# Kernel optimization log

Measured on AMD Instinct MI355X. Metric: run time of the kernel, lower is better.

The kernel has to match this reference:

```python
import jax, jax.numpy as jnp
from jax import lax
import numpy as np

B, T, D, H, K = 16, 2048, 512, 512, 2

def setup_inputs() -> dict:
    key = jax.random.key(0)
    k1, k2, k3 = jax.random.split(key, 3)
    inputs = jax.random.normal(k1, (B, T, D), dtype=jnp.float32)
    conv_w = jax.random.normal(k2, (3 * H, D, K), dtype=jnp.float32) * (1.0 / np.sqrt(D * K))
    conv_b = jax.random.normal(k3, (3 * H,), dtype=jnp.float32) * 0.01
    return {"inputs": inputs, "conv_w": conv_w, "conv_b": conv_b}

def reference(inputs, conv_w, conv_b):
    # inputs: [B, T, D]; conv_w: [3H, D, K]; causal conv via left-pad K-1
    k = conv_w.shape[-1]
    h = conv_w.shape[0] // 3
    x = jnp.transpose(inputs, (0, 2, 1))                      # [B, D, T]
    x = jnp.pad(x, ((0, 0), (0, 0), (k - 1, 0)))              # left pad
    gates = lax.conv_general_dilated(
        x, conv_w, window_strides=(1,), padding='VALID',
        dimension_numbers=('NCH', 'OIH', 'NCH'))              # [B, 3H, T]
    gates = jnp.transpose(gates, (0, 2, 1)) + conv_b          # [B, T, 3H]
    Z, F, O = jnp.split(gates, 3, axis=2)
    Z = jnp.tanh(Z)
    F = jax.nn.sigmoid(F)
    O = jax.nn.sigmoid(O)

    # fo-pool: c_t = f_t * c_{t-1} + (1 - f_t) * z_t, c_{-1} = 0
    def step(c, zf):
        z, f = zf
        c_ = f * c + (1.0 - f) * z
        return c_, c_

    c0 = jnp.zeros((Z.shape[0], h), dtype=Z.dtype)
    _, C = lax.scan(step, c0, (jnp.swapaxes(Z, 0, 1), jnp.swapaxes(F, 0, 1)))
    C = jnp.swapaxes(C, 0, 1)                                 # [B, T, H]
    return C, O * C
```

## Files before the change

### kernel.cpp

```cpp
#include <hip/hip_runtime.h>


#define MTOT 32768
#define NTOT 1536
#define KTOT 1024
#define DCH  512
#define TLEN 2048
#define NB   16

#define HT 32
#define SC 8
#define LC 256

typedef __bf16 bf16x8 __attribute__((ext_vector_type(8)));
typedef float  f32x4  __attribute__((ext_vector_type(4)));

__device__ __forceinline__ unsigned short f2bf(float x) {
    unsigned u = __float_as_uint(x);
    u += 0x7FFFu + ((u >> 16) & 1u);
    return (unsigned short)(u >> 16);
}
__device__ __forceinline__ float bf2f(unsigned short h) {
    return __uint_as_float(((unsigned)h) << 16);
}
__device__ __forceinline__ float sigmoidf_(float x) {
    return 1.f / (1.f + __expf(-x));
}

__global__ __launch_bounds__(256) void make_A(const float* __restrict__ in,
                                              unsigned short* __restrict__ A) {
    size_t i = (size_t)blockIdx.x * 256 + threadIdx.x;
    size_t e = i * 8;
    size_t m = e >> 10;
    int    j = (int)(e & 1023);
    alignas(16) unsigned short h[8];
    if (((m & (TLEN - 1)) == 0) && (j < DCH)) {
#pragma unroll
        for (int r = 0; r < 8; ++r) h[r] = 0;
    } else {
        const float* src = in + ((long long)m - 1) * DCH + j;
        float4 a = *(const float4*)src;
        float4 b = *(const float4*)(src + 4);
        h[0] = f2bf(a.x); h[1] = f2bf(a.y); h[2] = f2bf(a.z); h[3] = f2bf(a.w);
        h[4] = f2bf(b.x); h[5] = f2bf(b.y); h[6] = f2bf(b.z); h[7] = f2bf(b.w);
    }
    *(int4*)(A + e) = *(const int4*)h;
}

__global__ __launch_bounds__(256) void make_B(const float* __restrict__ w,
                                              unsigned short* __restrict__ Bt) {
    int i = blockIdx.x * 256 + threadIdx.x;
    int o = i >> 9, d = i & 511;
    float w0 = w[(size_t)(o * 512 + d) * 2];
    float w1 = w[(size_t)(o * 512 + d) * 2 + 1];
    Bt[(size_t)o * 1024 + d]       = f2bf(w0);
    Bt[(size_t)o * 1024 + 512 + d] = f2bf(w1);
}

__global__ __launch_bounds__(256) void gemm_gates(const unsigned short* __restrict__ A,
                                                  const unsigned short* __restrict__ B,
                                                  const float* __restrict__ bias,
                                                  unsigned short* __restrict__ GT) {
    __shared__ int4 sA[512];
    __shared__ int4 sB[512];

    const int tid = threadIdx.x;
    const int bx  = blockIdx.x;
    const int mT  = bx / 12, nT = bx % 12;
    const int m0  = mT * 128, n0 = nT * 128;

    const int mloc = tid >> 2;
    const int qsw  = (tid & 3) ^ ((mloc >> 1) & 3);
    const unsigned short* ga0 = A + (size_t)(m0 + mloc) * 1024 + qsw * 8;
    const unsigned short* ga1 = A + (size_t)(m0 + 64 + mloc) * 1024 + qsw * 8;
    const unsigned short* gb0 = B + (size_t)(n0 + mloc) * 1024 + qsw * 8;
    const unsigned short* gb1 = B + (size_t)(n0 + 64 + mloc) * 1024 + qsw * 8;

    char* la0 = (char*)sA + tid * 16;
    char* la1 = (char*)sA + 4096 + tid * 16;
    char* lb0 = (char*)sB + tid * 16;
    char* lb1 = (char*)sB + 4096 + tid * 16;

    const int lane = tid & 63;
    const int wv   = tid >> 6;
    const int wm   = (wv & 1) * 64, wn = (wv >> 1) * 64;
    const int lr   = lane & 15, lq = lane >> 4;

    int sAidx[4], sBidx[4];
#pragma unroll
    for (int i = 0; i < 4; ++i) {
        int mi = wm + 16 * i + lr;
        sAidx[i] = mi * 4 + (lq ^ ((mi >> 1) & 3));
        int ni = wn + 16 * i + lr;
        sBidx[i] = ni * 4 + (lq ^ ((ni >> 1) & 3));
    }

    f32x4 acc[4][4] = {};

    for (int kt = 0; kt < KTOT; kt += 32) {
        __builtin_amdgcn_global_load_lds(
            (__attribute__((address_space(1))) void*)(void*)ga0,
            (__attribute__((address_space(3))) void*)la0, 16, 0, 0);
        __builtin_amdgcn_global_load_lds(
            (__attribute__((address_space(1))) void*)(void*)ga1,
            (__attribute__((address_space(3))) void*)la1, 16, 0, 0);
        __builtin_amdgcn_global_load_lds(
            (__attribute__((address_space(1))) void*)(void*)gb0,
            (__attribute__((address_space(3))) void*)lb0, 16, 0, 0);
        __builtin_amdgcn_global_load_lds(
            (__attribute__((address_space(1))) void*)(void*)gb1,
            (__attribute__((address_space(3))) void*)lb1, 16, 0, 0);
        ga0 += 32; ga1 += 32; gb0 += 32; gb1 += 32;
        __syncthreads();

        bf16x8 af[4], bfr[4];
#pragma unroll
        for (int i = 0; i < 4; ++i) af[i]  = __builtin_bit_cast(bf16x8, sA[sAidx[i]]);
#pragma unroll
        for (int j = 0; j < 4; ++j) bfr[j] = __builtin_bit_cast(bf16x8, sB[sBidx[j]]);

#pragma unroll
        for (int i = 0; i < 4; ++i)
#pragma unroll
            for (int j = 0; j < 4; ++j)
                acc[i][j] = __builtin_amdgcn_mfma_f32_16x16x32_bf16(af[i], bfr[j],
                                                                    acc[i][j], 0, 0, 0);
        __syncthreads();
    }

#pragma unroll
    for (int j = 0; j < 4; ++j) {
        int gn = n0 + wn + 16 * j + lr;
        float bj = bias[gn];
#pragma unroll
        for (int i = 0; i < 4; ++i) {
            int rowb = m0 + wm + 16 * i + lq * 4;
            alignas(8) unsigned short pk[4];
#pragma unroll
            for (int r = 0; r < 4; ++r) pk[r] = f2bf(acc[i][j][r] + bj);
            *(int2*)(GT + (size_t)gn * MTOT + rowb) = *(const int2*)pk;
        }
    }
}

__global__ __launch_bounds__(256) void scan_fo(const unsigned short* __restrict__ GT,
                                               float* __restrict__ out) {
    __shared__ float lP[SC][HT];
    __shared__ float lC[SC][HT];
    __shared__ float lI[SC][HT];

    const int tid   = threadIdx.x;
    const int h_loc = tid & (HT - 1);
    const int s     = tid >> 5;
    const int b     = blockIdx.x >> 4;
    const int h0    = (blockIdx.x & 15) * HT;
    const int h     = h0 + h_loc;

    const size_t mbase = (size_t)b * TLEN + (size_t)s * LC;
    const unsigned short* gz = GT + (size_t)h * MTOT + mbase;
    const unsigned short* gf = GT + (size_t)(DCH + h) * MTOT + mbase;
    const unsigned short* go = GT + (size_t)(2 * DCH + h) * MTOT + mbase;

    float P = 1.f, c = 0.f;
    for (int k = 0; k < LC; k += 8) {
        bf16x8 zv = *(const bf16x8*)(gz + k);
        bf16x8 fv = *(const bf16x8*)(gf + k);
#pragma unroll
        for (int r = 0; r < 8; ++r) {
            float f = sigmoidf_((float)fv[r]);
            float z = 2.f * sigmoidf_(2.f * (float)zv[r]) - 1.f;
            c = f * c + (1.f - f) * z;
            P *= f;
        }
    }
    lP[s][h_loc] = P;
    lC[s][h_loc] = c;
    __syncthreads();

    if (tid < HT) {
        float cc = 0.f;
#pragma unroll
        for (int ss = 0; ss < SC; ++ss) {
            lI[ss][tid] = cc;
            cc = lP[ss][tid] * cc + lC[ss][tid];
        }
    }
    __syncthreads();

    c = lI[s][h_loc];
    const size_t BTH = (size_t)NB * TLEN * DCH;
    float* oC  = out + mbase * DCH + h;
    float* oOC = oC + BTH;
    for (int k = 0; k < LC; k += 8) {
        bf16x8 zv = *(const bf16x8*)(gz + k);
        bf16x8 fv = *(const bf16x8*)(gf + k);
        bf16x8 ov = *(const bf16x8*)(go + k);
#pragma unroll
        for (int r = 0; r < 8; ++r) {
            float f = sigmoidf_((float)fv[r]);
            float z = 2.f * sigmoidf_(2.f * (float)zv[r]) - 1.f;
            float o = sigmoidf_((float)ov[r]);
            c = f * c + (1.f - f) * z;
            oC[(size_t)(k + r) * DCH]  = c;
            oOC[(size_t)(k + r) * DCH] = o * c;
        }
    }
}

extern "C" void kernel_launch(void* const* d_in, const int* in_sizes, int n_in,
                              void* d_out, int out_size, void* d_ws, size_t ws_size,
                              hipStream_t stream) {
    const float* in   = (const float*)d_in[0];
    const float* w    = (const float*)d_in[1];
    const float* bias = (const float*)d_in[2];
    float* out = (float*)d_out;

    unsigned short* Abf = (unsigned short*)d_ws;
    unsigned short* Bbf = Abf + (size_t)MTOT * 1024;
    unsigned short* GT  = Bbf + (size_t)NTOT * 1024;

    make_A<<<dim3(16384), dim3(256), 0, stream>>>(in, Abf);
    make_B<<<dim3(3072),  dim3(256), 0, stream>>>(w, Bbf);
    gemm_gates<<<dim3(3072), dim3(256), 0, stream>>>(Abf, Bbf, bias, GT);
    scan_fo<<<dim3(NB * (DCH / HT)), dim3(256), 0, stream>>>(GT, out);
}
```

Measured before the change: 407.7 us.

## Split fo-pool scan into three kernels with shorter chunks and remap GEMM blocks

The single scan kernel used 256 blocks, each walking 256-step chunks. It is replaced by three kernels: per-chunk prefix products and states over 64-step chunks (1024 blocks), a cross-chunk carry scan over 32 chunks per chain, and a final pass that writes the outputs. The point is more parallelism and shorter serial dependency chains in the recurrence, paid for with two extra launches and a small workspace round-trip. The workspace reuses the bf16 A buffer, which is dead once the GEMM finishes. The GEMM block index is also permuted so that neighbouring blocks land on different tile groups, which may change L2 locality.

```diff
diff --git a/kernel.cpp b/kernel.cpp
--- a/kernel.cpp
+++ b/kernel.cpp
@@ -8,9 +8,9 @@
 #define TLEN 2048
 #define NB   16
 
-#define HT 32
-#define SC 8
-#define LC 256
+#define LC2    64
+#define NCH    32
+#define CHAINS 8192
 
 typedef __bf16 bf16x8 __attribute__((ext_vector_type(8)));
 typedef float  f32x4  __attribute__((ext_vector_type(4)));
@@ -65,7 +65,8 @@
     __shared__ int4 sB[512];
 
     const int tid = threadIdx.x;
-    const int bx  = blockIdx.x;
+    const int bx0 = blockIdx.x;
+    const int bx  = (bx0 & 7) * 384 + (bx0 >> 3);
     const int mT  = bx / 12, nT = bx % 12;
     const int m0  = mT * 128, n0 = nT * 128;
 
@@ -143,26 +144,25 @@
     }
 }
 
-__global__ __launch_bounds__(256) void scan_fo(const unsigned short* __restrict__ GT,
-                                               float* __restrict__ out) {
-    __shared__ float lP[SC][HT];
-    __shared__ float lC[SC][HT];
-    __shared__ float lI[SC][HT];
-
+__global__ __launch_bounds__(256) void scan_part1(const unsigned short* __restrict__ GT,
+                                                  float* __restrict__ Pws,
+                                                  float* __restrict__ Cws) {
     const int tid   = threadIdx.x;
-    const int h_loc = tid & (HT - 1);
-    const int s     = tid >> 5;
-    const int b     = blockIdx.x >> 4;
-    const int h0    = (blockIdx.x & 15) * HT;
-    const int h     = h0 + h_loc;
-
-    const size_t mbase = (size_t)b * TLEN + (size_t)s * LC;
+    const int h_loc = tid & 31;
+    const int sc    = tid >> 5;
+    const int bid   = blockIdx.x;
+    const int tg    = bid & 3;
+    const int hg    = (bid >> 2) & 15;
+    const int b     = bid >> 6;
+    const int h     = hg * 32 + h_loc;
+    const int cg    = tg * 8 + sc;
+
+    const size_t mbase = (size_t)b * TLEN + (size_t)cg * LC2;
     const unsigned short* gz = GT + (size_t)h * MTOT + mbase;
     const unsigned short* gf = GT + (size_t)(DCH + h) * MTOT + mbase;
-    const unsigned short* go = GT + (size_t)(2 * DCH + h) * MTOT + mbase;
 
     float P = 1.f, c = 0.f;
-    for (int k = 0; k < LC; k += 8) {
+    for (int k = 0; k < LC2; k += 8) {
         bf16x8 zv = *(const bf16x8*)(gz + k);
         bf16x8 fv = *(const bf16x8*)(gf + k);
 #pragma unroll
@@ -173,25 +173,49 @@
             P *= f;
         }
     }
-    lP[s][h_loc] = P;
-    lC[s][h_loc] = c;
-    __syncthreads();
-
-    if (tid < HT) {
-        float cc = 0.f;
-#pragma unroll
-        for (int ss = 0; ss < SC; ++ss) {
-            lI[ss][tid] = cc;
-            cc = lP[ss][tid] * cc + lC[ss][tid];
-        }
-    }
-    __syncthreads();
-
-    c = lI[s][h_loc];
+    const int ch = b * DCH + h;
+    Pws[(size_t)cg * CHAINS + ch] = P;
+    Cws[(size_t)cg * CHAINS + ch] = c;
+}
+
+__global__ __launch_bounds__(256) void scan_part2(const float* __restrict__ Pws,
+                                                  const float* __restrict__ Cws,
+                                                  float* __restrict__ Iws) {
+    const int ch = blockIdx.x * 256 + threadIdx.x;
+    float cc = 0.f;
+#pragma unroll
+    for (int cg = 0; cg < NCH; ++cg) {
+        size_t idx = (size_t)cg * CHAINS + ch;
+        Iws[idx] = cc;
+        cc = Pws[idx] * cc + Cws[idx];
+    }
+}
+
+__global__ __launch_bounds__(256) void scan_part3(const unsigned short* __restrict__ GT,
+                                                  const float* __restrict__ Iws,
+                                                  float* __restrict__ out) {
+    const int tid   = threadIdx.x;
+    const int h_loc = tid & 31;
+    const int sc    = tid >> 5;
+    const int bid   = blockIdx.x;
+    const int tg    = bid & 3;
+    const int hg    = (bid >> 2) & 15;
+    const int b     = bid >> 6;
+    const int h     = hg * 32 + h_loc;
+    const int cg    = tg * 8 + sc;
+
+    const size_t mbase = (size_t)b * TLEN + (size_t)cg * LC2;
+    const unsigned short* gz = GT + (size_t)h * MTOT + mbase;
+    const unsigned short* gf = GT + (size_t)(DCH + h) * MTOT + mbase;
+    const unsigned short* go = GT + (size_t)(2 * DCH + h) * MTOT + mbase;
+
+    const int ch = b * DCH + h;
+    float c = Iws[(size_t)cg * CHAINS + ch];
+
     const size_t BTH = (size_t)NB * TLEN * DCH;
     float* oC  = out + mbase * DCH + h;
     float* oOC = oC + BTH;
-    for (int k = 0; k < LC; k += 8) {
+    for (int k = 0; k < LC2; k += 8) {
         bf16x8 zv = *(const bf16x8*)(gz + k);
         bf16x8 fv = *(const bf16x8*)(gf + k);
         bf16x8 ov = *(const bf16x8*)(go + k);
@@ -219,8 +243,14 @@
     unsigned short* Bbf = Abf + (size_t)MTOT * 1024;
     unsigned short* GT  = Bbf + (size_t)NTOT * 1024;
 
+    float* Pws = (float*)d_ws;
+    float* Cws = Pws + (size_t)NCH * CHAINS;
+    float* Iws = Cws + (size_t)NCH * CHAINS;
+
     make_A<<<dim3(16384), dim3(256), 0, stream>>>(in, Abf);
     make_B<<<dim3(3072),  dim3(256), 0, stream>>>(w, Bbf);
     gemm_gates<<<dim3(3072), dim3(256), 0, stream>>>(Abf, Bbf, bias, GT);
-    scan_fo<<<dim3(NB * (DCH / HT)), dim3(256), 0, stream>>>(GT, out);
-}
+    scan_part1<<<dim3(1024), dim3(256), 0, stream>>>(GT, Pws, Cws);
+    scan_part2<<<dim3(CHAINS / 256), dim3(256), 0, stream>>>(Pws, Cws, Iws);
+    scan_part3<<<dim3(1024), dim3(256), 0, stream>>>(GT, Iws, out);
+}
```

Result: slower. 517.4 us (+26.9%).
